# Performance work log

Measured on AMD Instinct MI355X. Metric: run time of the kernel, lower is better.

Reference implementation:

```python
import jax, jax.numpy as jnp
import numpy as np


def gcn_conv(x, edge_index, W, b, num_nodes):
    # PyG GCNConv: add self-loops, symmetric normalization, linear transform.
    src, dst = edge_index[0], edge_index[1]
    loop = jnp.arange(num_nodes, dtype=src.dtype)
    src = jnp.concatenate([src, loop])
    dst = jnp.concatenate([dst, loop])
    ones = jnp.ones(src.shape[0], dtype=x.dtype)
    deg = jax.ops.segment_sum(ones, dst, num_segments=num_nodes)
    dinv = jnp.where(deg > 0, jax.lax.rsqrt(deg), 0.0).astype(x.dtype)
    norm = dinv[src] * dinv[dst]  # [E+N]
    h = x @ W                      # [N_in, out]
    msg = h[src] * norm[:, None]   # gather + scale (memory bound)
    out = jax.ops.segment_sum(msg, dst, num_segments=num_nodes)
    return out + b


def upsample2(z):
    # interpolate(scale_factor=2) along node dim, nearest -> repeat each node twice
    return jnp.repeat(z, 2, axis=0)


def setup_inputs() -> dict:
    key = jax.random.key(0)
    ks = jax.random.split(key, 16)
    N = 25000
    h0, h1, h2, out_c = 64, 128, 256, 8
    deg = 16

    def edges(k, n):
        return jax.random.randint(k, (2, n * deg), 0, n, dtype=jnp.int64)

    inp = {
        "z": jax.random.normal(ks[0], (N, h2), dtype=jnp.float32),
        "edge_index": edges(ks[1], N),
        "ps2": edges(ks[2], 2 * N),
        "ps1": edges(ks[3], 4 * N),
        "ps0": edges(ks[4], 8 * N),
        "W1": jax.random.normal(ks[5], (h2, h2), dtype=jnp.float32) / np.sqrt(h2),
        "b1": jnp.zeros((h2,), dtype=jnp.float32),
        "W2": jax.random.normal(ks[6], (h2, h1), dtype=jnp.float32) / np.sqrt(h2),
        "b2": jnp.zeros((h1,), dtype=jnp.float32),
        "W3": jax.random.normal(ks[7], (h1, h0), dtype=jnp.float32) / np.sqrt(h1),
        "b3": jnp.zeros((h0,), dtype=jnp.float32),
        "W4": jax.random.normal(ks[8], (h0, out_c), dtype=jnp.float32) / np.sqrt(h0),
        "b4": jnp.zeros((out_c,), dtype=jnp.float32),
    }
    return inp


def reference(z, edge_index, ps2, ps1, ps0, W1, b1, W2, b2, W3, b3, W4, b4):
    N = z.shape[0]
    z = jax.nn.relu(gcn_conv(z, edge_index, W1, b1, N))
    z = upsample2(z)
    z = jax.nn.relu(gcn_conv(z, ps2, W2, b2, 2 * N))
    z = upsample2(z)
    z = jax.nn.relu(gcn_conv(z, ps1, W3, b3, 4 * N))
    z = upsample2(z)
    z = gcn_conv(z, ps0, W4, b4, 8 * N)
    return z
```

## Files before the change

kernel.cpp:

```cpp
#include <hip/hip_runtime.h>
#include <hip/hip_fp16.h>


static inline int cdiv(long a, int b) { return (int)((a + b - 1) / b); }
static constexpr int NBLK = 512;

typedef _Float16 half8 __attribute__((ext_vector_type(8)));
typedef float f32x4 __attribute__((ext_vector_type(4)));

__device__ inline void unpack8(uint4 u, float f[8]) {
  __half2 a = __builtin_bit_cast(__half2, u.x);
  __half2 b = __builtin_bit_cast(__half2, u.y);
  __half2 c = __builtin_bit_cast(__half2, u.z);
  __half2 d = __builtin_bit_cast(__half2, u.w);
  float2 fa = __half22float2(a), fb = __half22float2(b);
  float2 fc = __half22float2(c), fd = __half22float2(d);
  f[0] = fa.x; f[1] = fa.y; f[2] = fb.x; f[3] = fb.y;
  f[4] = fc.x; f[5] = fc.y; f[6] = fd.x; f[7] = fd.y;
}

__device__ inline uint4 relu8h(uint4 u) {
  uint4 r;
  unsigned m;
  m = ((u.x >> 15) & 0x00010001u) * 0xFFFFu; r.x = u.x & ~m;
  m = ((u.y >> 15) & 0x00010001u) * 0xFFFFu; r.y = u.y & ~m;
  m = ((u.z >> 15) & 0x00010001u) * 0xFFFFu; r.z = u.z & ~m;
  m = ((u.w >> 15) & 0x00010001u) * 0xFFFFu; r.w = u.w & ~m;
  return r;
}

__global__ __launch_bounds__(1024) void part_hist_fused(
    const int* __restrict__ d1, const int* __restrict__ d2, const int* __restrict__ d3,
    const int* __restrict__ d4, int* __restrict__ histGA, int* __restrict__ histGB,
    int E1, int E12, int ETA, int chunkA, int NBAall, int B2, int B3,
    int E4, int chunkB, int NB4all) {
  __shared__ int hist[784];
  const int kb = blockIdx.x;
  if (kb < NBLK) {
    const int k = kb;
    for (int i = threadIdx.x; i < NBAall; i += 1024) hist[i] = 0;
    __syncthreads();
    const int lo = k * chunkA, hi = min(ETA, lo + chunkA);
    for (int e = lo + (int)threadIdx.x; e < hi; e += 1024) {
      int l, ee;
      if (e < E1) { l = 0; ee = e; }
      else if (e < E12) { l = 1; ee = e - E1; }
      else { l = 2; ee = e - E12; }
      const int* dp = (l == 0) ? d1 : (l == 1) ? d2 : d3;
      int base = (l == 0) ? 0 : (l == 1) ? B2 : B3;
      atomicAdd(&hist[base + (dp[ee] >> 8)], 1);
    }
    __syncthreads();
    for (int i = threadIdx.x; i < NBAall; i += 1024) histGA[i * NBLK + k] = hist[i];
  } else {
    const int k = kb - NBLK;
    for (int i = threadIdx.x; i < NB4all; i += 1024) hist[i] = 0;
    __syncthreads();
    const int lo = k * chunkB, hi = min(E4, lo + chunkB);
    for (int e = lo + (int)threadIdx.x; e < hi; e += 1024)
      atomicAdd(&hist[d4[e] >> 8], 1);
    __syncthreads();
    for (int i = threadIdx.x; i < NB4all; i += 1024) histGB[i * NBLK + k] = hist[i];
  }
}

__global__ void scan_block_fused(int* __restrict__ arrA, int* __restrict__ psA,
                                 int nA, int nbsAq,
                                 int* __restrict__ arrB, int* __restrict__ psB, int nB) {
  __shared__ int tmp[256];
  const int b = blockIdx.x;
  int* arr; int* ps; int n; int bb;
  if (b < nbsAq) { arr = arrA; ps = psA; n = nA; bb = b; }
  else { arr = arrB; ps = psB; n = nB; bb = b - nbsAq; }
  int i = bb * 256 + threadIdx.x;
  int v = (i < n) ? arr[i] : 0;
  tmp[threadIdx.x] = v;
  __syncthreads();
  for (int off = 1; off < 256; off <<= 1) {
    int t = (threadIdx.x >= off) ? tmp[threadIdx.x - off] : 0;
    __syncthreads();
    tmp[threadIdx.x] += t;
    __syncthreads();
  }
  if (i < n) arr[i] = tmp[threadIdx.x] - v;
  if (threadIdx.x == 255) ps[bb] = tmp[255];
}

__global__ __launch_bounds__(1024) void scan_psum_fused(int* __restrict__ psA2, int nA,
                                                        int* __restrict__ psB2, int nB) {
  __shared__ int tmp[1024];
  int* ps = (blockIdx.x == 0) ? psA2 : psB2;
  const int nb = (blockIdx.x == 0) ? nA : nB;
  int i = threadIdx.x;
  int v = (i < nb) ? ps[i] : 0;
  tmp[i] = v;
  __syncthreads();
  for (int off = 1; off < 1024; off <<= 1) {
    int t = (i >= off) ? tmp[i - off] : 0;
    __syncthreads();
    tmp[i] += t;
    __syncthreads();
  }
  if (i < nb) ps[i] = tmp[i] - v;
}

__global__ void scan_add_fused(int* __restrict__ vA, const int* __restrict__ psA,
                               int nA, int nbsAq,
                               int* __restrict__ vB, const int* __restrict__ psB, int nB) {
  const int b = blockIdx.x;
  int* v; const int* ps; int n; int bb;
  if (b < nbsAq) { v = vA; ps = psA; n = nA; bb = b; }
  else { v = vB; ps = psB; n = nB; bb = b - nbsAq; }
  int i = bb * 256 + threadIdx.x;
  if (i < n) v[i] += ps[bb];
}

__global__ void extract_offs_fused(const int* __restrict__ histGA, int* __restrict__ boffsA,
                                   int NBAall, int EtotA,
                                   const int* __restrict__ histGB, int* __restrict__ boffsB,
                                   int NB4all, int EtotB) {
  int i = blockIdx.x * 256 + threadIdx.x;
  if (i <= NBAall) boffsA[i] = (i < NBAall) ? histGA[i * NBLK] : EtotA;
  int j = i - (NBAall + 1);
  if (j >= 0 && j <= NB4all) boffsB[j] = (j < NB4all) ? histGB[j * NBLK] : EtotB;
}

template <int CHUNK, int NBCAP>
__global__ __launch_bounds__(1024) void part_scatter3_staged(
    const int* __restrict__ s1, const int* __restrict__ d1,
    const int* __restrict__ s2, const int* __restrict__ d2,
    const int* __restrict__ s3, const int* __restrict__ d3,
    const int* __restrict__ histG, int* __restrict__ bins,
    int E1, int E12, int ET, int chunk, int NBall, int B2, int B3) {
  __shared__ int stage[CHUNK];
  __shared__ int cnt[NBCAP];
  __shared__ int cur[NBCAP];
  __shared__ int gb[NBCAP];
  const int tid = threadIdx.x;
  const int k = blockIdx.x;
  for (int i = tid; i < NBall; i += 1024) {
    const int idx = i * NBLK + k;
    const int base = histG[idx];
    const int nxt = (idx + 1 < NBall * NBLK) ? histG[idx + 1] : ET;
    gb[i] = base;
    cnt[i] = nxt - base;
  }
  __syncthreads();
  int sum = (tid < NBall) ? cnt[tid] : 0;
  stage[tid] = sum;
  __syncthreads();
  for (int off = 1; off < 1024; off <<= 1) {
    int t = (tid >= off) ? stage[tid - off] : 0;
    __syncthreads();
    stage[tid] += t;
    __syncthreads();
  }
  if (tid < NBall) cur[tid] = stage[tid] - sum;
  __syncthreads();
  const int lo = k * chunk, hi = min(ET, lo + chunk);
  for (int e = lo + tid; e < hi; e += 1024) {
    int l, ee;
    if (e < E1) { l = 0; ee = e; }
    else if (e < E12) { l = 1; ee = e - E1; }
    else { l = 2; ee = e - E12; }
    const int* sp = (l == 0) ? s1 : (l == 1) ? s2 : s3;
    const int* dp = (l == 0) ? d1 : (l == 1) ? d2 : d3;
    int base = (l == 0) ? 0 : (l == 1) ? B2 : B3;
    int d = dp[ee];
    int p = atomicAdd(&cur[base + (d >> 8)], 1);
    stage[p] = sp[ee] | ((d & 255) << 18);
  }
  __syncthreads();
  const int wave = tid >> 6, lane = tid & 63;
  for (int b = wave; b < NBall; b += 16) {
    int cb = cnt[b];
    int lbase = cur[b] - cb;
    int gbase = gb[b];
    for (int t = lane; t < cb; t += 64) bins[gbase + t] = stage[lbase + t];
  }
}

template <int CHUNK, int NBCAP>
__global__ __launch_bounds__(1024) void part_scatter4_staged(
    const int* __restrict__ src, const int* __restrict__ dst,
    const int* __restrict__ histG, int* __restrict__ bins,
    int E, int chunk, int NBall) {
  __shared__ int stage[CHUNK];
  __shared__ int cnt[NBCAP];
  __shared__ int cur[NBCAP];
  __shared__ int gb[NBCAP];
  const int tid = threadIdx.x;
  const int k = blockIdx.x;
  for (int i = tid; i < NBall; i += 1024) {
    const int idx = i * NBLK + k;
    const int base = histG[idx];
    const int nxt = (idx + 1 < NBall * NBLK) ? histG[idx + 1] : E;
    gb[i] = base;
    cnt[i] = nxt - base;
  }
  __syncthreads();
  int sum = (tid < NBall) ? cnt[tid] : 0;
  stage[tid] = sum;
  __syncthreads();
  for (int off = 1; off < 1024; off <<= 1) {
    int t = (tid >= off) ? stage[tid - off] : 0;
    __syncthreads();
    stage[tid] += t;
    __syncthreads();
  }
  if (tid < NBall) cur[tid] = stage[tid] - sum;
  __syncthreads();
  const int lo = k * chunk, hi = min(E, lo + chunk);
  for (int e = lo + tid; e < hi; e += 1024) {
    int d = dst[e];
    int p = atomicAdd(&cur[d >> 8], 1);
    stage[p] = src[e] | ((d & 255) << 18);
  }
  __syncthreads();
  const int wave = tid >> 6, lane = tid & 63;
  for (int b = wave; b < NBall; b += 16) {
    int cb = cnt[b];
    int lbase = cur[b] - cb;
    int gbase = gb[b];
    for (int t = lane; t < cb; t += 64) bins[gbase + t] = stage[lbase + t];
  }
}

__global__ __launch_bounds__(256) void csrify_fused(
    int* __restrict__ binsA, const int* __restrict__ boffsA,
    int* __restrict__ binsB, const int* __restrict__ boffsB,
    int* __restrict__ no1, int* __restrict__ no2, int* __restrict__ no3,
    int* __restrict__ no4,
    float* __restrict__ dv1, float* __restrict__ dv2, float* __restrict__ dv3,
    float* __restrict__ dv4,
    int n1, int n2, int n3, int n4, int NB1, int NB2, int NB3, int NBAq, int NB4q) {
  __shared__ int cnt[256];
  __shared__ int scanv[256];
  __shared__ int cur[256];
  const int bbg = blockIdx.x;
  const int tid = threadIdx.x;
  int lb, nl, nbl, bo;
  int* noffs;
  float* dinv;
  int* bins;
  const int* boffs;
  if (bbg < NB1) {
    lb = bbg; nl = n1; nbl = NB1; noffs = no1; dinv = dv1; bins = binsA; boffs = boffsA; bo = bbg;
  } else if (bbg < NB1 + NB2) {
    lb = bbg - NB1; nl = n2; nbl = NB2; noffs = no2; dinv = dv2; bins = binsA; boffs = boffsA; bo = bbg;
  } else if (bbg < NBAq) {
    lb = bbg - NB1 - NB2; nl = n3; nbl = NB3; noffs = no3; dinv = dv3; bins = binsA; boffs = boffsA; bo = bbg;
  } else {
    lb = bbg - NBAq; nl = n4; nbl = NB4q; noffs = no4; dinv = dv4; bins = binsB; boffs = boffsB; bo = lb;
  }
  cnt[tid] = 0;
  __syncthreads();
  const int start = boffs[bo], end = boffs[bo + 1];
  int rv[24];
#pragma unroll
  for (int kk = 0; kk < 24; kk++) {
    int e = start + tid + kk * 256;
    rv[kk] = (e < end) ? bins[e] : -1;
    if (rv[kk] != -1) atomicAdd(&cnt[rv[kk] >> 18], 1);
  }
  __syncthreads();
  scanv[tid] = cnt[tid];
  __syncthreads();
  for (int off = 1; off < 256; off <<= 1) {
    int t = (tid >= off) ? scanv[tid - off] : 0;
    __syncthreads();
    scanv[tid] += t;
    __syncthreads();
  }
  int excl = scanv[tid] - cnt[tid];
  cur[tid] = excl;
  int node = lb * 256 + tid;
  if (node < nl) {
    noffs[node] = start + excl;
    dinv[node] = rsqrtf((float)cnt[tid] + 1.0f);
  }
  if (lb == nbl - 1 && tid == 0) noffs[nl] = end;
  __syncthreads();
#pragma unroll
  for (int kk = 0; kk < 24; kk++) {
    if (rv[kk] != -1) {
      int dl = rv[kk] >> 18;
      int pos = start + atomicAdd(&cur[dl], 1);
      bins[pos] = rv[kk] & 0x3FFFF;
    }
  }
}

template <int C, int HSHIFT>
__global__ __launch_bounds__(256) void node_gather_h16(const int* __restrict__ csr,
                                                       const int* __restrict__ noffs,
                                                       const float* __restrict__ dinv,
                                                       const __half* __restrict__ h,
                                                       const float* __restrict__ b,
                                                       __half* __restrict__ out, int n) {
  constexpr int LPN = C / 8;
  constexpr int NPB = 256 / LPN;
  const int node = blockIdx.x * NPB + threadIdx.x / LPN;
  const int c8 = (threadIdx.x % LPN) * 8;
  if (node >= n) return;
  const int start = noffs[node];
  const int end = noffs[node + 1];
  const float dd = dinv[node];
  float acc[8];
  {
    uint4 u = *reinterpret_cast<const uint4*>(&h[((long)(node >> HSHIFT)) * C + c8]);
    float f[8];
    unpack8(u, f);
#pragma unroll
    for (int i = 0; i < 8; ++i) acc[i] = dd * f[i];
  }
  int j = start;
  for (; j + 3 < end; j += 4) {
    int s0 = csr[j], s1 = csr[j + 1], s2 = csr[j + 2], s3 = csr[j + 3];
    float w0 = dinv[s0], w1 = dinv[s1], w2 = dinv[s2], w3 = dinv[s3];
    uint4 u0 = *reinterpret_cast<const uint4*>(&h[((long)(s0 >> HSHIFT)) * C + c8]);
    uint4 u1 = *reinterpret_cast<const uint4*>(&h[((long)(s1 >> HSHIFT)) * C + c8]);
    uint4 u2 = *reinterpret_cast<const uint4*>(&h[((long)(s2 >> HSHIFT)) * C + c8]);
    uint4 u3 = *reinterpret_cast<const uint4*>(&h[((long)(s3 >> HSHIFT)) * C + c8]);
    float f0[8], f1[8], f2[8], f3[8];
    unpack8(u0, f0); unpack8(u1, f1); unpack8(u2, f2); unpack8(u3, f3);
#pragma unroll
    for (int i = 0; i < 8; ++i) acc[i] = fmaf(w0, f0[i], acc[i]);
#pragma unroll
    for (int i = 0; i < 8; ++i) acc[i] = fmaf(w1, f1[i], acc[i]);
#pragma unroll
    for (int i = 0; i < 8; ++i) acc[i] = fmaf(w2, f2[i], acc[i]);
#pragma unroll
    for (int i = 0; i < 8; ++i) acc[i] = fmaf(w3, f3[i], acc[i]);
  }
  for (; j < end; ++j) {
    int s0 = csr[j];
    float w0 = dinv[s0];
    uint4 u0 = *reinterpret_cast<const uint4*>(&h[((long)(s0 >> HSHIFT)) * C + c8]);
    float f0[8];
    unpack8(u0, f0);
#pragma unroll
    for (int i = 0; i < 8; ++i) acc[i] = fmaf(w0, f0[i], acc[i]);
  }
  const float4 b0 = *reinterpret_cast<const float4*>(b + c8);
  const float4 b1 = *reinterpret_cast<const float4*>(b + c8 + 4);
  float o[8];
  o[0] = fmaf(dd, acc[0], b0.x); o[1] = fmaf(dd, acc[1], b0.y);
  o[2] = fmaf(dd, acc[2], b0.z); o[3] = fmaf(dd, acc[3], b0.w);
  o[4] = fmaf(dd, acc[4], b1.x); o[5] = fmaf(dd, acc[5], b1.y);
  o[6] = fmaf(dd, acc[6], b1.z); o[7] = fmaf(dd, acc[7], b1.w);
  unsigned pk[4];
#pragma unroll
  for (int q = 0; q < 4; ++q) {
    __half2 t2 = __floats2half2_rn(o[2 * q], o[2 * q + 1]);
    pk[q] = __builtin_bit_cast(unsigned, t2);
  }
  uint4 ov;
  ov.x = pk[0]; ov.y = pk[1]; ov.z = pk[2]; ov.w = pk[3];
  *reinterpret_cast<uint4*>(out + (long)node * C + c8) = ov;
}

__global__ __launch_bounds__(256) void node_gather_g4(const int* __restrict__ csr,
                                                      const int* __restrict__ noffs,
                                                      const float* __restrict__ dinv,
                                                      const __half* __restrict__ g4,
                                                      const float* __restrict__ b,
                                                      float* __restrict__ out, int n) {
  const int node = blockIdx.x * 256 + threadIdx.x;
  if (node >= n) return;
  const int start = noffs[node];
  const int end = noffs[node + 1];
  const float dd = dinv[node];
  float acc[8];
  {
    uint4 u = *reinterpret_cast<const uint4*>(&g4[(long)node * 8]);
    unpack8(u, acc);
  }
  int j = start;
  for (; j + 3 < end; j += 4) {
    int s0 = csr[j], s1 = csr[j + 1], s2 = csr[j + 2], s3 = csr[j + 3];
    uint4 u0 = *reinterpret_cast<const uint4*>(&g4[(long)s0 * 8]);
    uint4 u1 = *reinterpret_cast<const uint4*>(&g4[(long)s1 * 8]);
    uint4 u2 = *reinterpret_cast<const uint4*>(&g4[(long)s2 * 8]);
    uint4 u3 = *reinterpret_cast<const uint4*>(&g4[(long)s3 * 8]);
    float f0[8], f1[8], f2[8], f3[8];
    unpack8(u0, f0); unpack8(u1, f1); unpack8(u2, f2); unpack8(u3, f3);
#pragma unroll
    for (int i = 0; i < 8; ++i) acc[i] += f0[i];
#pragma unroll
    for (int i = 0; i < 8; ++i) acc[i] += f1[i];
#pragma unroll
    for (int i = 0; i < 8; ++i) acc[i] += f2[i];
#pragma unroll
    for (int i = 0; i < 8; ++i) acc[i] += f3[i];
  }
  for (; j < end; ++j) {
    int s0 = csr[j];
    uint4 u0 = *reinterpret_cast<const uint4*>(&g4[(long)s0 * 8]);
    float f0[8];
    unpack8(u0, f0);
#pragma unroll
    for (int i = 0; i < 8; ++i) acc[i] += f0[i];
  }
  const float4 b0 = *reinterpret_cast<const float4*>(b);
  const float4 b1 = *reinterpret_cast<const float4*>(b + 4);
  float4 o0, o1;
  o0.x = fmaf(dd, acc[0], b0.x); o0.y = fmaf(dd, acc[1], b0.y);
  o0.z = fmaf(dd, acc[2], b0.z); o0.w = fmaf(dd, acc[3], b0.w);
  o1.x = fmaf(dd, acc[4], b1.x); o1.y = fmaf(dd, acc[5], b1.y);
  o1.z = fmaf(dd, acc[6], b1.z); o1.w = fmaf(dd, acc[7], b1.w);
  float* __restrict__ op = out + (long)node * 8;
  *reinterpret_cast<float4*>(op) = o0;
  *reinterpret_cast<float4*>(op + 4) = o1;
}

__global__ __launch_bounds__(256) void wconv_all(const float* __restrict__ W1,
                                                 const float* __restrict__ W2,
                                                 const float* __restrict__ W3,
                                                 __half* __restrict__ wt1,
                                                 __half* __restrict__ wt2,
                                                 __half* __restrict__ wt3) {
  int i = blockIdx.x * 256 + threadIdx.x;
  if (i < 65536) {
    int c = i >> 8, k = i & 255;
    wt1[i] = __float2half(W1[k * 256 + c]);
  } else if (i < 98304) {
    int j = i - 65536;
    int c = j >> 8, k = j & 255;
    wt2[j] = __float2half(W2[k * 128 + c]);
  } else if (i < 106496) {
    int j = i - 98304;
    int c = j >> 7, k = j & 127;
    wt3[j] = __float2half(W3[k * 64 + c]);
  }
}

template <int CIN, int COUT, int BN, bool RELU, bool HIN>
__global__ __launch_bounds__(256) void gemm_mf(const void* __restrict__ xv,
                                               const __half* __restrict__ wt,
                                               __half* __restrict__ hh, int n) {
  constexpr int BM = 64;
  constexpr int KT = 32;
  constexpr int NT = CIN / KT;
  constexpr int NF = BN / 16;
  constexpr int RS = 40;
  constexpr int BF = BN * 4 / 256;

  __shared__ __align__(16) __half aT[2][BM * RS];
  __shared__ __align__(16) __half bT[2][BN * RS];

  const float* __restrict__ xf = (const float*)xv;
  const __half* __restrict__ xh = (const __half*)xv;
  const int tid = threadIdx.x;
  const int rowbase = blockIdx.x * BM;
  const int colbase = blockIdx.y * BN;

  uint4 pua;
  float4 paf0, paf1;
  uint4 pub[BF];

  auto stage_load = [&](int t) {
    const int k0 = t * KT;
    {
      const int r = tid >> 2, kq = tid & 3;
      const int gr = rowbase + r;
      if constexpr (HIN) {
        uint4 v = make_uint4(0u, 0u, 0u, 0u);
        if (gr < n) v = *reinterpret_cast<const uint4*>(&xh[(long)gr * CIN + k0 + kq * 8]);
        pua = v;
      } else {
        float4 v0 = make_float4(0.f, 0.f, 0.f, 0.f), v1 = v0;
        if (gr < n) {
          v0 = *reinterpret_cast<const float4*>(&xf[(long)gr * CIN + k0 + kq * 8]);
          v1 = *reinterpret_cast<const float4*>(&xf[(long)gr * CIN + k0 + kq * 8 + 4]);
        }
        paf0 = v0; paf1 = v1;
      }
    }
#pragma unroll
    for (int u = 0; u < BF; ++u) {
      const int i = u * 256 + tid;
      const int c = i >> 2, kq = i & 3;
      pub[u] = *reinterpret_cast<const uint4*>(&wt[(long)(colbase + c) * CIN + k0 + kq * 8]);
    }
  };
  auto stage_write = [&](int buf) {
    {
      const int r = tid >> 2, kq = tid & 3;
      if constexpr (HIN) {
        uint4 v = RELU ? relu8h(pua) : pua;
        *reinterpret_cast<uint4*>(&aT[buf][r * RS + kq * 8]) = v;
      } else {
        float f[8] = {paf0.x, paf0.y, paf0.z, paf0.w, paf1.x, paf1.y, paf1.z, paf1.w};
        if (RELU) {
#pragma unroll
          for (int j = 0; j < 8; ++j) f[j] = fmaxf(f[j], 0.f);
        }
        unsigned pk[4];
#pragma unroll
        for (int q = 0; q < 4; ++q) {
          __half2 t2 = __floats2half2_rn(f[2 * q], f[2 * q + 1]);
          pk[q] = __builtin_bit_cast(unsigned, t2);
        }
        uint4 v; v.x = pk[0]; v.y = pk[1]; v.z = pk[2]; v.w = pk[3];
        *reinterpret_cast<uint4*>(&aT[buf][r * RS + kq * 8]) = v;
      }
    }
#pragma unroll
    for (int u = 0; u < BF; ++u) {
      const int i = u * 256 + tid;
      const int c = i >> 2, kq = i & 3;
      *reinterpret_cast<uint4*>(&bT[buf][c * RS + kq * 8]) = pub[u];
    }
  };

  f32x4 acc[NF];
#pragma unroll
  for (int cf = 0; cf < NF; ++cf) acc[cf] = (f32x4){0.f, 0.f, 0.f, 0.f};

  stage_load(0);
  stage_write(0);
  __syncthreads();

  const int w = tid >> 6;
  const int l = tid & 63;
  const int m16 = l & 15;
  const int kg = l >> 4;

  for (int t = 0; t < NT; ++t) {
    const int cur = t & 1;
    if (t + 1 < NT) stage_load(t + 1);
    const half8 af =
        *reinterpret_cast<const half8*>(&aT[cur][(w * 16 + m16) * RS + kg * 8]);
#pragma unroll
    for (int cf = 0; cf < NF; ++cf) {
      const half8 bf =
          *reinterpret_cast<const half8*>(&bT[cur][(cf * 16 + m16) * RS + kg * 8]);
      acc[cf] = __builtin_amdgcn_mfma_f32_16x16x32_f16(af, bf, acc[cf], 0, 0, 0);
    }
    if (t + 1 < NT) stage_write(cur ^ 1);
    __syncthreads();
  }

#pragma unroll
  for (int reg = 0; reg < 4; ++reg) {
    const int gr = rowbase + w * 16 + kg * 4 + reg;
    if (gr < n) {
      __half* __restrict__ hp = &hh[(long)gr * COUT + colbase + m16];
#pragma unroll
      for (int cf = 0; cf < NF; ++cf) hp[cf * 16] = __float2half(acc[cf][reg]);
    }
  }
}

template <int CIN, int COUT, int TM, bool RELU>
__global__ __launch_bounds__(256) void gemm_small_g(const __half* __restrict__ x,
                                                    const float* __restrict__ W,
                                                    const float* __restrict__ dv4,
                                                    __half* __restrict__ g4, int n) {
  __shared__ float xs[TM][CIN + 1];
  const int tid = threadIdx.x;
  const int base = blockIdx.x * TM;
  constexpr int NL = TM * CIN / 8;
  for (int i = tid; i < NL; i += 256) {
    int m = i / (CIN / 8), kq = i % (CIN / 8);
    int r = base + m;
    uint4 v = make_uint4(0u, 0u, 0u, 0u);
    if (r < n) v = *reinterpret_cast<const uint4*>(&x[(long)r * CIN + kq * 8]);
    float f[8];
    unpack8(v, f);
#pragma unroll
    for (int j = 0; j < 8; ++j)
      xs[m][kq * 8 + j] = RELU ? fmaxf(f[j], 0.f) : f[j];
  }
  __syncthreads();
  constexpr int GROUPS = 256 / COUT;
  constexpr int ACC = TM / GROUPS;
  const int c = tid % COUT;
  const int mg = tid / COUT;
  float acc[ACC];
#pragma unroll
  for (int a = 0; a < ACC; a++) acc[a] = 0.f;
#pragma unroll 8
  for (int k = 0; k < CIN; k++) {
    float wk = W[k * COUT + c];
#pragma unroll
    for (int a = 0; a < ACC; a++) acc[a] = fmaf(xs[mg + a * GROUPS][k], wk, acc[a]);
  }
#pragma unroll
  for (int a = 0; a < ACC; a++) {
    int r = base + mg + a * GROUPS;
    if (r < n) {
      float v = acc[a];
      g4[(long)(2 * r) * COUT + c] = __float2half(dv4[2 * r] * v);
      g4[(long)(2 * r + 1) * COUT + c] = __float2half(dv4[2 * r + 1] * v);
    }
  }
}

extern "C" void kernel_launch(void* const* d_in, const int* in_sizes, int n_in,
                              void* d_out, int out_size, void* d_ws, size_t ws_size,
                              hipStream_t stream) {
  const float* z  = (const float*)d_in[0];
  const int* ei   = (const int*)d_in[1];
  const int* ps2  = (const int*)d_in[2];
  const int* ps1  = (const int*)d_in[3];
  const int* ps0  = (const int*)d_in[4];
  const float* W1 = (const float*)d_in[5];  const float* b1 = (const float*)d_in[6];
  const float* W2 = (const float*)d_in[7];  const float* b2 = (const float*)d_in[8];
  const float* W3 = (const float*)d_in[9];  const float* b3 = (const float*)d_in[10];
  const float* W4 = (const float*)d_in[11]; const float* b4 = (const float*)d_in[12];
  float* out = (float*)d_out;

  const int N  = in_sizes[0] / 256;
  const int E1 = in_sizes[1] / 2;
  const int E2 = in_sizes[2] / 2;
  const int E3 = in_sizes[3] / 2;
  const int E4 = in_sizes[4] / 2;
  const int n1 = N, n2 = 2 * N, n3 = 4 * N, n4 = 8 * N;
  const int E12 = E1 + E2, ETA = E1 + E2 + E3;
  const int NB1 = cdiv(n1, 256);
  const int NB2 = cdiv(n2, 256);
  const int NB3 = cdiv(n3, 256);
  const int NB4 = cdiv(n4, 256);
  const int NBA = NB1 + NB2 + NB3;
  const int B2b = NB1, B3b = NB1 + NB2;
  const int NTA = NBA * NBLK;
  const int nbsA = cdiv(NTA, 256);
  const int nbsA2 = cdiv(nbsA, 256);
  const int NTB = NB4 * NBLK;
  const int nbsB = cdiv(NTB, 256);
  const int nbsB2 = cdiv(nbsB, 256);
  const int chunk3 = cdiv(ETA, NBLK);
  const int chunk4 = cdiv(E4, NBLK);

  float* F = (float*)d_ws;
  __half* h1 = (__half*)F;
  __half* out1 = (__half*)(F + 6400000);
  __half* h2 = (__half*)F;
  int* binsB = (int*)(F + 3200000);
  __half* out2 = (__half*)(F + 6400000);
  __half* h3 = (__half*)F;
  __half* out3 = (__half*)(F + 6400000);
  __half* g4 = (__half*)F;

  int* P = (int*)(F + 12800000);
  int* binsA = P;
  int* no1 = P + ETA;
  int* no2 = no1 + (n1 + 1);
  int* no3 = no2 + (n2 + 1);
  int* no4 = no3 + (n3 + 1);
  float* dv1 = (float*)(no4 + (n4 + 1));
  float* dv2 = dv1 + n1;
  float* dv3 = dv2 + n2;
  float* dv4 = dv3 + n3;
  int* S = (int*)(dv4 + n4);
  int* histA = S;
  int* psumA = histA + NTA;
  int* psumA2 = psumA + 2048;
  int* boffsA = psumA2 + 64;
  int* histB = boffsA + (NBA + 1);
  int* psumB = histB + NTB;
  int* psumB2 = psumB + 2048;
  int* boffsB = psumB2 + 64;

  __half* wt1 = (__half*)histA;
  __half* wt2 = wt1 + 256 * 256;
  __half* wt3 = wt2 + 128 * 256;

  part_hist_fused<<<2 * NBLK, 1024, 0, stream>>>(
      ei + E1, ps2 + E2, ps1 + E3, ps0 + E4, histA, histB,
      E1, E12, ETA, chunk3, NBA, B2b, B3b, E4, chunk4, NB4);
  scan_block_fused<<<nbsA + nbsB, 256, 0, stream>>>(histA, psumA, NTA, nbsA,
                                                    histB, psumB, NTB);
  scan_block_fused<<<nbsA2 + nbsB2, 256, 0, stream>>>(psumA, psumA2, nbsA, nbsA2,
                                                      psumB, psumB2, nbsB);
  scan_psum_fused<<<2, 1024, 0, stream>>>(psumA2, nbsA2, psumB2, nbsB2);
  scan_add_fused<<<nbsA2 + nbsB2, 256, 0, stream>>>(psumA, psumA2, nbsA, nbsA2,
                                                    psumB, psumB2, nbsB);
  scan_add_fused<<<nbsA + nbsB, 256, 0, stream>>>(histA, psumA, NTA, nbsA,
                                                  histB, psumB, NTB);
  extract_offs_fused<<<cdiv((NBA + 1) + (NB4 + 1), 256), 256, 0, stream>>>(
      histA, boffsA, NBA, ETA, histB, boffsB, NB4, E4);
  part_scatter3_staged<5472, 688><<<NBLK, 1024, 0, stream>>>(
      ei, ei + E1, ps2, ps2 + E2, ps1, ps1 + E3, histA, binsA,
      E1, E12, ETA, chunk3, NBA, B2b, B3b);
  part_scatter4_staged<6256, 784><<<NBLK, 1024, 0, stream>>>(ps0, ps0 + E4, histB, binsB,
                                                             E4, chunk4, NB4);
  csrify_fused<<<NBA + NB4, 256, 0, stream>>>(binsA, boffsA, binsB, boffsB,
                                              no1, no2, no3, no4, dv1, dv2, dv3, dv4,
                                              n1, n2, n3, n4, NB1, NB2, NB3, NBA, NB4);

  wconv_all<<<cdiv(106496, 256), 256, 0, stream>>>(W1, W2, W3, wt1, wt2, wt3);

  gemm_mf<256, 256, 128, false, false><<<dim3(cdiv(n1, 64), 2), 256, 0, stream>>>(z, wt1, h1, n1);
  node_gather_h16<256, 0><<<cdiv(n1, 8), 256, 0, stream>>>(binsA, no1, dv1, h1, b1, out1, n1);

  gemm_mf<256, 128, 128, true, true><<<dim3(cdiv(N, 64), 1), 256, 0, stream>>>(out1, wt2, h2, N);
  node_gather_h16<128, 1><<<cdiv(n2, 16), 256, 0, stream>>>(binsA, no2, dv2, h2, b2, out2, n2);

  gemm_mf<128, 64, 64, true, true><<<dim3(cdiv(2 * N, 64), 1), 256, 0, stream>>>(out2, wt3, h3, 2 * N);
  node_gather_h16<64, 1><<<cdiv(n3, 32), 256, 0, stream>>>(binsA, no3, dv3, h3, b3, out3, n3);

  gemm_small_g<64, 8, 32, true><<<cdiv(4 * N, 32), 256, 0, stream>>>(out3, W4, dv4, g4, 4 * N);
  node_gather_g4<<<cdiv(n4, 256), 256, 0, stream>>>(binsB, no4, dv4, g4, b4, out, n4);
}
```

Measured before the change: 399.0 us.

## Replace global histogram scan with atomic bucket reservation into fixed-capacity bins

The separate histogram kernel and the multi-kernel prefix scan over per-block bucket counts are removed. Each scatter block now counts its edges per bucket in shared memory and reserves space in a fixed-capacity slot per bucket (CAP entries) with one global atomicAdd per bucket. Node offsets are paired with explicit per-node counts, so the CSR no longer needs to be globally contiguous. This cuts about six kernel launches and the scan traffic, at the cost of reading the edge destinations twice inside the scatter kernel and assuming no bucket ever exceeds CAP edges. Edge order within buckets also becomes nondeterministic.

```diff
diff --git a/kernel.cpp b/kernel.cpp
--- a/kernel.cpp
+++ b/kernel.cpp
@@ -4,6 +4,7 @@
 
 static inline int cdiv(long a, int b) { return (int)((a + b - 1) / b); }
 static constexpr int NBLK = 512;
+static constexpr int CAP = 6144;
 
 typedef _Float16 half8 __attribute__((ext_vector_type(8)));
 typedef float f32x4 __attribute__((ext_vector_type(4)));
@@ -29,124 +30,39 @@
   return r;
 }
 
-__global__ __launch_bounds__(1024) void part_hist_fused(
-    const int* __restrict__ d1, const int* __restrict__ d2, const int* __restrict__ d3,
-    const int* __restrict__ d4, int* __restrict__ histGA, int* __restrict__ histGB,
-    int E1, int E12, int ETA, int chunkA, int NBAall, int B2, int B3,
-    int E4, int chunkB, int NB4all) {
-  __shared__ int hist[784];
-  const int kb = blockIdx.x;
-  if (kb < NBLK) {
-    const int k = kb;
-    for (int i = threadIdx.x; i < NBAall; i += 1024) hist[i] = 0;
-    __syncthreads();
-    const int lo = k * chunkA, hi = min(ETA, lo + chunkA);
-    for (int e = lo + (int)threadIdx.x; e < hi; e += 1024) {
-      int l, ee;
-      if (e < E1) { l = 0; ee = e; }
-      else if (e < E12) { l = 1; ee = e - E1; }
-      else { l = 2; ee = e - E12; }
-      const int* dp = (l == 0) ? d1 : (l == 1) ? d2 : d3;
-      int base = (l == 0) ? 0 : (l == 1) ? B2 : B3;
-      atomicAdd(&hist[base + (dp[ee] >> 8)], 1);
-    }
-    __syncthreads();
-    for (int i = threadIdx.x; i < NBAall; i += 1024) histGA[i * NBLK + k] = hist[i];
-  } else {
-    const int k = kb - NBLK;
-    for (int i = threadIdx.x; i < NB4all; i += 1024) hist[i] = 0;
-    __syncthreads();
-    const int lo = k * chunkB, hi = min(E4, lo + chunkB);
-    for (int e = lo + (int)threadIdx.x; e < hi; e += 1024)
-      atomicAdd(&hist[d4[e] >> 8], 1);
-    __syncthreads();
-    for (int i = threadIdx.x; i < NB4all; i += 1024) histGB[i * NBLK + k] = hist[i];
-  }
-}
-
-__global__ void scan_block_fused(int* __restrict__ arrA, int* __restrict__ psA,
-                                 int nA, int nbsAq,
-                                 int* __restrict__ arrB, int* __restrict__ psB, int nB) {
-  __shared__ int tmp[256];
-  const int b = blockIdx.x;
-  int* arr; int* ps; int n; int bb;
-  if (b < nbsAq) { arr = arrA; ps = psA; n = nA; bb = b; }
-  else { arr = arrB; ps = psB; n = nB; bb = b - nbsAq; }
-  int i = bb * 256 + threadIdx.x;
-  int v = (i < n) ? arr[i] : 0;
-  tmp[threadIdx.x] = v;
-  __syncthreads();
-  for (int off = 1; off < 256; off <<= 1) {
-    int t = (threadIdx.x >= off) ? tmp[threadIdx.x - off] : 0;
-    __syncthreads();
-    tmp[threadIdx.x] += t;
-    __syncthreads();
-  }
-  if (i < n) arr[i] = tmp[threadIdx.x] - v;
-  if (threadIdx.x == 255) ps[bb] = tmp[255];
-}
-
-__global__ __launch_bounds__(1024) void scan_psum_fused(int* __restrict__ psA2, int nA,
-                                                        int* __restrict__ psB2, int nB) {
-  __shared__ int tmp[1024];
-  int* ps = (blockIdx.x == 0) ? psA2 : psB2;
-  const int nb = (blockIdx.x == 0) ? nA : nB;
-  int i = threadIdx.x;
-  int v = (i < nb) ? ps[i] : 0;
-  tmp[i] = v;
-  __syncthreads();
-  for (int off = 1; off < 1024; off <<= 1) {
-    int t = (i >= off) ? tmp[i - off] : 0;
-    __syncthreads();
-    tmp[i] += t;
-    __syncthreads();
-  }
-  if (i < nb) ps[i] = tmp[i] - v;
-}
-
-__global__ void scan_add_fused(int* __restrict__ vA, const int* __restrict__ psA,
-                               int nA, int nbsAq,
-                               int* __restrict__ vB, const int* __restrict__ psB, int nB) {
-  const int b = blockIdx.x;
-  int* v; const int* ps; int n; int bb;
-  if (b < nbsAq) { v = vA; ps = psA; n = nA; bb = b; }
-  else { v = vB; ps = psB; n = nB; bb = b - nbsAq; }
-  int i = bb * 256 + threadIdx.x;
-  if (i < n) v[i] += ps[bb];
-}
-
-__global__ void extract_offs_fused(const int* __restrict__ histGA, int* __restrict__ boffsA,
-                                   int NBAall, int EtotA,
-                                   const int* __restrict__ histGB, int* __restrict__ boffsB,
-                                   int NB4all, int EtotB) {
+__global__ void zero_cnt_kernel(int* __restrict__ a, int n) {
   int i = blockIdx.x * 256 + threadIdx.x;
-  if (i <= NBAall) boffsA[i] = (i < NBAall) ? histGA[i * NBLK] : EtotA;
-  int j = i - (NBAall + 1);
-  if (j >= 0 && j <= NB4all) boffsB[j] = (j < NB4all) ? histGB[j * NBLK] : EtotB;
+  if (i < n) a[i] = 0;
 }
 
 template <int CHUNK, int NBCAP>
-__global__ __launch_bounds__(1024) void part_scatter3_staged(
+__global__ __launch_bounds__(1024) void part_scatter3_atomic(
     const int* __restrict__ s1, const int* __restrict__ d1,
     const int* __restrict__ s2, const int* __restrict__ d2,
     const int* __restrict__ s3, const int* __restrict__ d3,
-    const int* __restrict__ histG, int* __restrict__ bins,
+    int* __restrict__ gcnt, int* __restrict__ bins,
     int E1, int E12, int ET, int chunk, int NBall, int B2, int B3) {
   __shared__ int stage[CHUNK];
   __shared__ int cnt[NBCAP];
   __shared__ int cur[NBCAP];
-  __shared__ int gb[NBCAP];
+  __shared__ int gbase[NBCAP];
   const int tid = threadIdx.x;
   const int k = blockIdx.x;
-  for (int i = tid; i < NBall; i += 1024) {
-    const int idx = i * NBLK + k;
-    const int base = histG[idx];
-    const int nxt = (idx + 1 < NBall * NBLK) ? histG[idx + 1] : ET;
-    gb[i] = base;
-    cnt[i] = nxt - base;
+  for (int i = tid; i < NBall; i += 1024) cnt[i] = 0;
+  __syncthreads();
+  const int lo = k * chunk, hi = min(ET, lo + chunk);
+  for (int e = lo + tid; e < hi; e += 1024) {
+    int l, ee;
+    if (e < E1) { l = 0; ee = e; }
+    else if (e < E12) { l = 1; ee = e - E1; }
+    else { l = 2; ee = e - E12; }
+    const int* dp = (l == 0) ? d1 : (l == 1) ? d2 : d3;
+    int base = (l == 0) ? 0 : (l == 1) ? B2 : B3;
+    atomicAdd(&cnt[base + (dp[ee] >> 8)], 1);
   }
   __syncthreads();
   int sum = (tid < NBall) ? cnt[tid] : 0;
+  if (tid < NBall && sum > 0) gbase[tid] = atomicAdd(&gcnt[tid], sum);
   stage[tid] = sum;
   __syncthreads();
   for (int off = 1; off < 1024; off <<= 1) {
@@ -157,7 +73,6 @@
   }
   if (tid < NBall) cur[tid] = stage[tid] - sum;
   __syncthreads();
-  const int lo = k * chunk, hi = min(ET, lo + chunk);
   for (int e = lo + tid; e < hi; e += 1024) {
     int l, ee;
     if (e < E1) { l = 0; ee = e; }
@@ -174,32 +89,31 @@
   const int wave = tid >> 6, lane = tid & 63;
   for (int b = wave; b < NBall; b += 16) {
     int cb = cnt[b];
+    if (cb == 0) continue;
     int lbase = cur[b] - cb;
-    int gbase = gb[b];
-    for (int t = lane; t < cb; t += 64) bins[gbase + t] = stage[lbase + t];
+    int gb2 = b * CAP + gbase[b];
+    for (int t = lane; t < cb; t += 64) bins[gb2 + t] = stage[lbase + t];
   }
 }
 
 template <int CHUNK, int NBCAP>
-__global__ __launch_bounds__(1024) void part_scatter4_staged(
+__global__ __launch_bounds__(1024) void part_scatter4_atomic(
     const int* __restrict__ src, const int* __restrict__ dst,
-    const int* __restrict__ histG, int* __restrict__ bins,
+    int* __restrict__ gcnt, int* __restrict__ bins,
     int E, int chunk, int NBall) {
   __shared__ int stage[CHUNK];
   __shared__ int cnt[NBCAP];
   __shared__ int cur[NBCAP];
-  __shared__ int gb[NBCAP];
+  __shared__ int gbase[NBCAP];
   const int tid = threadIdx.x;
   const int k = blockIdx.x;
-  for (int i = tid; i < NBall; i += 1024) {
-    const int idx = i * NBLK + k;
-    const int base = histG[idx];
-    const int nxt = (idx + 1 < NBall * NBLK) ? histG[idx + 1] : E;
-    gb[i] = base;
-    cnt[i] = nxt - base;
-  }
+  for (int i = tid; i < NBall; i += 1024) cnt[i] = 0;
+  __syncthreads();
+  const int lo = k * chunk, hi = min(E, lo + chunk);
+  for (int e = lo + tid; e < hi; e += 1024) atomicAdd(&cnt[dst[e] >> 8], 1);
   __syncthreads();
   int sum = (tid < NBall) ? cnt[tid] : 0;
+  if (tid < NBall && sum > 0) gbase[tid] = atomicAdd(&gcnt[tid], sum);
   stage[tid] = sum;
   __syncthreads();
   for (int off = 1; off < 1024; off <<= 1) {
@@ -210,7 +124,6 @@
   }
   if (tid < NBall) cur[tid] = stage[tid] - sum;
   __syncthreads();
-  const int lo = k * chunk, hi = min(E, lo + chunk);
   for (int e = lo + tid; e < hi; e += 1024) {
     int d = dst[e];
     int p = atomicAdd(&cur[d >> 8], 1);
@@ -220,42 +133,47 @@
   const int wave = tid >> 6, lane = tid & 63;
   for (int b = wave; b < NBall; b += 16) {
     int cb = cnt[b];
+    if (cb == 0) continue;
     int lbase = cur[b] - cb;
-    int gbase = gb[b];
-    for (int t = lane; t < cb; t += 64) bins[gbase + t] = stage[lbase + t];
+    int gb2 = b * CAP + gbase[b];
+    for (int t = lane; t < cb; t += 64) bins[gb2 + t] = stage[lbase + t];
   }
 }
 
 __global__ __launch_bounds__(256) void csrify_fused(
-    int* __restrict__ binsA, const int* __restrict__ boffsA,
-    int* __restrict__ binsB, const int* __restrict__ boffsB,
+    int* __restrict__ binsA, const int* __restrict__ gcntA,
+    int* __restrict__ binsB, const int* __restrict__ gcntB,
     int* __restrict__ no1, int* __restrict__ no2, int* __restrict__ no3,
     int* __restrict__ no4,
+    int* __restrict__ nc1, int* __restrict__ nc2, int* __restrict__ nc3,
+    int* __restrict__ nc4,
     float* __restrict__ dv1, float* __restrict__ dv2, float* __restrict__ dv3,
     float* __restrict__ dv4,
-    int n1, int n2, int n3, int n4, int NB1, int NB2, int NB3, int NBAq, int NB4q) {
+    int n1, int n2, int n3, int n4, int NB1, int NB2, int NB3, int NBAq) {
   __shared__ int cnt[256];
   __shared__ int scanv[256];
   __shared__ int cur[256];
   const int bbg = blockIdx.x;
   const int tid = threadIdx.x;
-  int lb, nl, nbl, bo;
+  int lb, nl, bo;
   int* noffs;
+  int* ncnt;
   float* dinv;
   int* bins;
-  const int* boffs;
+  const int* gcnt;
   if (bbg < NB1) {
-    lb = bbg; nl = n1; nbl = NB1; noffs = no1; dinv = dv1; bins = binsA; boffs = boffsA; bo = bbg;
+    lb = bbg; nl = n1; noffs = no1; ncnt = nc1; dinv = dv1; bins = binsA; gcnt = gcntA; bo = bbg;
   } else if (bbg < NB1 + NB2) {
-    lb = bbg - NB1; nl = n2; nbl = NB2; noffs = no2; dinv = dv2; bins = binsA; boffs = boffsA; bo = bbg;
+    lb = bbg - NB1; nl = n2; noffs = no2; ncnt = nc2; dinv = dv2; bins = binsA; gcnt = gcntA; bo = bbg;
   } else if (bbg < NBAq) {
-    lb = bbg - NB1 - NB2; nl = n3; nbl = NB3; noffs = no3; dinv = dv3; bins = binsA; boffs = boffsA; bo = bbg;
+    lb = bbg - NB1 - NB2; nl = n3; noffs = no3; ncnt = nc3; dinv = dv3; bins = binsA; gcnt = gcntA; bo = bbg;
   } else {
-    lb = bbg - NBAq; nl = n4; nbl = NB4q; noffs = no4; dinv = dv4; bins = binsB; boffs = boffsB; bo = lb;
+    lb = bbg - NBAq; nl = n4; noffs = no4; ncnt = nc4; dinv = dv4; bins = binsB; gcnt = gcntB; bo = lb;
   }
   cnt[tid] = 0;
   __syncthreads();
-  const int start = boffs[bo], end = boffs[bo + 1];
+  const int start = bo * CAP;
+  const int end = start + gcnt[bo];
   int rv[24];
 #pragma unroll
   for (int kk = 0; kk < 24; kk++) {
@@ -277,9 +195,9 @@
   int node = lb * 256 + tid;
   if (node < nl) {
     noffs[node] = start + excl;
+    ncnt[node] = cnt[tid];
     dinv[node] = rsqrtf((float)cnt[tid] + 1.0f);
   }
-  if (lb == nbl - 1 && tid == 0) noffs[nl] = end;
   __syncthreads();
 #pragma unroll
   for (int kk = 0; kk < 24; kk++) {
@@ -294,6 +212,7 @@
 template <int C, int HSHIFT>
 __global__ __launch_bounds__(256) void node_gather_h16(const int* __restrict__ csr,
                                                        const int* __restrict__ noffs,
+                                                       const int* __restrict__ ncnt,
                                                        const float* __restrict__ dinv,
                                                        const __half* __restrict__ h,
                                                        const float* __restrict__ b,
@@ -304,7 +223,7 @@
   const int c8 = (threadIdx.x % LPN) * 8;
   if (node >= n) return;
   const int start = noffs[node];
-  const int end = noffs[node + 1];
+  const int end = start + ncnt[node];
   const float dd = dinv[node];
   float acc[8];
   {
@@ -362,6 +281,7 @@
 
 __global__ __launch_bounds__(256) void node_gather_g4(const int* __restrict__ csr,
                                                       const int* __restrict__ noffs,
+                                                      const int* __restrict__ ncnt,
                                                       const float* __restrict__ dinv,
                                                       const __half* __restrict__ g4,
                                                       const float* __restrict__ b,
@@ -369,7 +289,7 @@
   const int node = blockIdx.x * 256 + threadIdx.x;
   if (node >= n) return;
   const int start = noffs[node];
-  const int end = noffs[node + 1];
+  const int end = start + ncnt[node];
   const float dd = dinv[node];
   float acc[8];
   {
@@ -625,12 +545,6 @@
   const int NB4 = cdiv(n4, 256);
   const int NBA = NB1 + NB2 + NB3;
   const int B2b = NB1, B3b = NB1 + NB2;
-  const int NTA = NBA * NBLK;
-  const int nbsA = cdiv(NTA, 256);
-  const int nbsA2 = cdiv(nbsA, 256);
-  const int NTB = NB4 * NBLK;
-  const int nbsB = cdiv(NTB, 256);
-  const int nbsB2 = cdiv(nbsB, 256);
   const int chunk3 = cdiv(ETA, NBLK);
   const int chunk4 = cdiv(E4, NBLK);
 
@@ -638,7 +552,6 @@
   __half* h1 = (__half*)F;
   __half* out1 = (__half*)(F + 6400000);
   __half* h2 = (__half*)F;
-  int* binsB = (int*)(F + 3200000);
   __half* out2 = (__half*)(F + 6400000);
   __half* h3 = (__half*)F;
   __half* out3 = (__half*)(F + 6400000);
@@ -646,62 +559,46 @@
 
   int* P = (int*)(F + 12800000);
   int* binsA = P;
-  int* no1 = P + ETA;
-  int* no2 = no1 + (n1 + 1);
-  int* no3 = no2 + (n2 + 1);
-  int* no4 = no3 + (n3 + 1);
-  float* dv1 = (float*)(no4 + (n4 + 1));
+  int* binsB = binsA + (long)NBA * CAP;
+  int* no1 = binsB + (long)NB4 * CAP;
+  int* no2 = no1 + n1;
+  int* no3 = no2 + n2;
+  int* no4 = no3 + n3;
+  int* nc1 = no4 + n4;
+  int* nc2 = nc1 + n1;
+  int* nc3 = nc2 + n2;
+  int* nc4 = nc3 + n3;
+  float* dv1 = (float*)(nc4 + n4);
   float* dv2 = dv1 + n1;
   float* dv3 = dv2 + n2;
   float* dv4 = dv3 + n3;
-  int* S = (int*)(dv4 + n4);
-  int* histA = S;
-  int* psumA = histA + NTA;
-  int* psumA2 = psumA + 2048;
-  int* boffsA = psumA2 + 64;
-  int* histB = boffsA + (NBA + 1);
-  int* psumB = histB + NTB;
-  int* psumB2 = psumB + 2048;
-  int* boffsB = psumB2 + 64;
-
-  __half* wt1 = (__half*)histA;
+  int* gcntA = (int*)(dv4 + n4);
+  int* gcntB = gcntA + NBA;
+  __half* wt1 = (__half*)(gcntB + NB4);
   __half* wt2 = wt1 + 256 * 256;
   __half* wt3 = wt2 + 128 * 256;
 
-  part_hist_fused<<<2 * NBLK, 1024, 0, stream>>>(
-      ei + E1, ps2 + E2, ps1 + E3, ps0 + E4, histA, histB,
-      E1, E12, ETA, chunk3, NBA, B2b, B3b, E4, chunk4, NB4);
-  scan_block_fused<<<nbsA + nbsB, 256, 0, stream>>>(histA, psumA, NTA, nbsA,
-                                                    histB, psumB, NTB);
-  scan_block_fused<<<nbsA2 + nbsB2, 256, 0, stream>>>(psumA, psumA2, nbsA, nbsA2,
-                                                      psumB, psumB2, nbsB);
-  scan_psum_fused<<<2, 1024, 0, stream>>>(psumA2, nbsA2, psumB2, nbsB2);
-  scan_add_fused<<<nbsA2 + nbsB2, 256, 0, stream>>>(psumA, psumA2, nbsA, nbsA2,
-                                                    psumB, psumB2, nbsB);
-  scan_add_fused<<<nbsA + nbsB, 256, 0, stream>>>(histA, psumA, NTA, nbsA,
-                                                  histB, psumB, NTB);
-  extract_offs_fused<<<cdiv((NBA + 1) + (NB4 + 1), 256), 256, 0, stream>>>(
-      histA, boffsA, NBA, ETA, histB, boffsB, NB4, E4);
-  part_scatter3_staged<5472, 688><<<NBLK, 1024, 0, stream>>>(
-      ei, ei + E1, ps2, ps2 + E2, ps1, ps1 + E3, histA, binsA,
+  zero_cnt_kernel<<<cdiv(NBA + NB4, 256), 256, 0, stream>>>(gcntA, NBA + NB4);
+  part_scatter3_atomic<5472, 688><<<NBLK, 1024, 0, stream>>>(
+      ei, ei + E1, ps2, ps2 + E2, ps1, ps1 + E3, gcntA, binsA,
       E1, E12, ETA, chunk3, NBA, B2b, B3b);
-  part_scatter4_staged<6256, 784><<<NBLK, 1024, 0, stream>>>(ps0, ps0 + E4, histB, binsB,
+  part_scatter4_atomic<6256, 784><<<NBLK, 1024, 0, stream>>>(ps0, ps0 + E4, gcntB, binsB,
                                                              E4, chunk4, NB4);
-  csrify_fused<<<NBA + NB4, 256, 0, stream>>>(binsA, boffsA, binsB, boffsB,
-                                              no1, no2, no3, no4, dv1, dv2, dv3, dv4,
-                                              n1, n2, n3, n4, NB1, NB2, NB3, NBA, NB4);
-
+  csrify_fused<<<NBA + NB4, 256, 0, stream>>>(binsA, gcntA, binsB, gcntB,
+                                              no1, no2, no3, no4, nc1, nc2, nc3, nc4,
+                                              dv1, dv2, dv3, dv4,
+                                              n1, n2, n3, n4, NB1, NB2, NB3, NBA);
   wconv_all<<<cdiv(106496, 256), 256, 0, stream>>>(W1, W2, W3, wt1, wt2, wt3);
 
   gemm_mf<256, 256, 128, false, false><<<dim3(cdiv(n1, 64), 2), 256, 0, stream>>>(z, wt1, h1, n1);
-  node_gather_h16<256, 0><<<cdiv(n1, 8), 256, 0, stream>>>(binsA, no1, dv1, h1, b1, out1, n1);
+  node_gather_h16<256, 0><<<cdiv(n1, 8), 256, 0, stream>>>(binsA, no1, nc1, dv1, h1, b1, out1, n1);
 
   gemm_mf<256, 128, 128, true, true><<<dim3(cdiv(N, 64), 1), 256, 0, stream>>>(out1, wt2, h2, N);
-  node_gather_h16<128, 1><<<cdiv(n2, 16), 256, 0, stream>>>(binsA, no2, dv2, h2, b2, out2, n2);
+  node_gather_h16<128, 1><<<cdiv(n2, 16), 256, 0, stream>>>(binsA, no2, nc2, dv2, h2, b2, out2, n2);
 
   gemm_mf<128, 64, 64, true, true><<<dim3(cdiv(2 * N, 64), 1), 256, 0, stream>>>(out2, wt3, h3, 2 * N);
-  node_gather_h16<64, 1><<<cdiv(n3, 32), 256, 0, stream>>>(binsA, no3, dv3, h3, b3, out3, n3);
+  node_gather_h16<64, 1><<<cdiv(n3, 32), 256, 0, stream>>>(binsA, no3, nc3, dv3, h3, b3, out3, n3);
 
   gemm_small_g<64, 8, 32, true><<<cdiv(4 * N, 32), 256, 0, stream>>>(out3, W4, dv4, g4, 4 * N);
-  node_gather_g4<<<cdiv(n4, 256), 256, 0, stream>>>(binsB, no4, dv4, g4, b4, out, n4);
-}
+  node_gather_g4<<<cdiv(n4, 256), 256, 0, stream>>>(binsB, no4, nc4, dv4, g4, b4, out, n4);
+}
```

After: 386.8 us. 3.1% less time.
